# Kernel optimization log

Hardware: AMD Instinct MI355X
Metric: run time of the kernel (lower is better)

The kernel has to match this reference:

```python
import jax, jax.numpy as jnp
import numpy as np

N_NODES = 50000
N_EDGES = 800000
HIDDEN = 128


def setup_inputs() -> dict:
    key = jax.random.key(0)
    k_emb, k_ei, k1, k2, k3, kb1, kb2, kb3 = jax.random.split(key, 8)
    emb = jax.random.normal(k_emb, (N_NODES, HIDDEN), dtype=jnp.float32)
    edge_index = jax.random.randint(k_ei, (2, N_EDGES), 0, N_NODES, dtype=jnp.int64)
    h = HIDDEN
    # MLP([2h, 4h, h, 1]) weights, Kaiming-uniform-ish init
    def lin(k, fan_in, fan_out):
        bound = 1.0 / np.sqrt(fan_in)
        return jax.random.uniform(k, (fan_in, fan_out), jnp.float32, -bound, bound)
    W1 = lin(k1, 2 * h, 4 * h)
    b1 = jax.random.uniform(kb1, (4 * h,), jnp.float32, -1.0 / np.sqrt(2 * h), 1.0 / np.sqrt(2 * h))
    W2 = lin(k2, 4 * h, h)
    b2 = jax.random.uniform(kb2, (h,), jnp.float32, -1.0 / np.sqrt(4 * h), 1.0 / np.sqrt(4 * h))
    W3 = lin(k3, h, 1)
    b3 = jax.random.uniform(kb3, (1,), jnp.float32, -1.0 / np.sqrt(h), 1.0 / np.sqrt(h))
    return {"emb": emb, "edge_index": edge_index,
            "W1": W1, "b1": b1, "W2": W2, "b2": b2, "W3": W3, "b3": b3}


def reference(emb, edge_index, W1, b1, W2, b2, W3, b3):
    # learn_edge_att=True path: gather endpoints, concat, 3-layer MLP
    col, row = edge_index[0], edge_index[1]
    f12 = jnp.concatenate([emb[col], emb[row]], axis=-1)  # [E, 2h]
    x = jax.nn.relu(f12 @ W1 + b1)                         # [E, 4h]
    x = jax.nn.relu(x @ W2 + b2)                           # [E, h]
    att_log_logits = x @ W3 + b3                           # [E, 1]
    return att_log_logits
```

## Files before the change

kernel.cpp:

```cpp
#include <hip/hip_runtime.h>
#include <hip/hip_bf16.h>
#include <stdint.h>

#define N_EDGES   800000
#define N_NODESC  50000
#define HID       128

typedef __attribute__((ext_vector_type(8))) short bf16x8;
typedef __attribute__((ext_vector_type(4))) float f32x4;
typedef __attribute__((ext_vector_type(4))) unsigned int u32x4;

__device__ __forceinline__ short f2bf(float f) {
    union { float f; uint32_t u; } v; v.f = f;
    uint32_t r = v.u + 0x7FFFu + ((v.u >> 16) & 1u);
    return (short)(r >> 16);
}

__device__ __forceinline__ uint32_t packbf2(float lo, float hi) {
    float2 t; t.x = lo; t.y = hi;
    __hip_bfloat162 h = __float22bfloat162_rn(t);
    uint32_t u;
    __builtin_memcpy(&u, &h, 4);
    return u;
}

__device__ __forceinline__ uint32_t addrelu2(uint32_t a, uint32_t b) {
    __hip_bfloat162 ha, hb;
    __builtin_memcpy(&ha, &a, 4);
    __builtin_memcpy(&hb, &b, 4);
    __hip_bfloat162 s = __hadd2(ha, hb);
    uint32_t x;
    __builtin_memcpy(&x, &s, 4);
    uint32_t neg = (x & 0x80008000u) >> 15;
    return x & ~(neg * 0xFFFFu);
}
__device__ __forceinline__ bf16x8 addrelu8(u32x4 p, u32x4 q) {
    u32x4 r;
    #pragma unroll
    for (int j = 0; j < 4; ++j) r[j] = addrelu2(p[j], q[j]);
    bf16x8 out;
    __builtin_memcpy(&out, &r, 16);
    return out;
}

#define PQ_OFF   0UL
#define W1S_OFF  102400000UL
#define W2S_OFF  (W1S_OFF + 262144UL)

__global__ __launch_bounds__(256) void swizzle_kernel(const float* __restrict__ W1,
                                                      const float* __restrict__ W2,
                                                      short* __restrict__ W1s,
                                                      short* __restrict__ W2s) {
    int t = blockIdx.x * 256 + threadIdx.x;
    int lane = t & 63;
    int kq = lane >> 4;
    int nn = lane & 15;
    if (t < 16384) {
        int frag = t >> 6;
        int kc = frag >> 6;
        int nt = frag & 63;
        int n = nt * 16 + nn;
        int kbase = kc * 32 + kq * 8;
        bf16x8 v;
        #pragma unroll
        for (int j = 0; j < 8; ++j) {
            int k = kbase + j;
            float f = (n < 512) ? W1[k * 512 + n] : W1[(128 + k) * 512 + (n - 512)];
            v[j] = f2bf(f);
        }
        *(bf16x8*)(W1s + frag * 512 + lane * 8) = v;
    } else if (t < 24576) {
        int t2 = t - 16384;
        int frag = t2 >> 6;
        int kc = frag >> 3;
        int nt = frag & 7;
        int n = nt * 16 + nn;
        int kbase = kc * 32 + kq * 8;
        bf16x8 v;
        #pragma unroll
        for (int j = 0; j < 8; ++j) v[j] = f2bf(W2[(kbase + j) * HID + n]);
        *(bf16x8*)(W2s + frag * 512 + lane * 8) = v;
    }
}

__global__ __launch_bounds__(256) void precompute_kernel(const float* __restrict__ emb,
                                                         const short* __restrict__ W1s,
                                                         const float* __restrict__ b1,
                                                         short* __restrict__ PQ) {
    __shared__ short tile[4][16][272];
    int lane = threadIdx.x & 63;
    int w = threadIdx.x >> 6;
    int nb = blockIdx.x * 16;
    int m = lane & 15;
    int kq = lane >> 4;

    const float* arow = emb + (size_t)(nb + m) * 128 + kq * 8;

    f32x4 acc[16];
    #pragma unroll
    for (int i = 0; i < 16; ++i) acc[i] = (f32x4){0.f, 0.f, 0.f, 0.f};

    #pragma unroll
    for (int kc = 0; kc < 4; ++kc) {
        f32x4 x0 = *(const f32x4*)(arow + kc * 32);
        f32x4 x1 = *(const f32x4*)(arow + kc * 32 + 4);
        u32x4 au;
        au[0] = packbf2(x0[0], x0[1]); au[1] = packbf2(x0[2], x0[3]);
        au[2] = packbf2(x1[0], x1[1]); au[3] = packbf2(x1[2], x1[3]);
        bf16x8 a;
        __builtin_memcpy(&a, &au, 16);
        #pragma unroll
        for (int nt = 0; nt < 16; ++nt) {
            int frag = kc * 64 + (w * 16 + nt);
            bf16x8 b = *(const bf16x8*)(W1s + frag * 512 + lane * 8);
            acc[nt] = __builtin_amdgcn_mfma_f32_16x16x32_bf16(a, b, acc[nt], 0, 0, 0);
        }
    }

    #pragma unroll
    for (int nt = 0; nt < 16; ++nt) {
        int n = w * 256 + nt * 16 + m;
        float bias = (n < 512) ? b1[n] : 0.0f;
        #pragma unroll
        for (int r = 0; r < 4; ++r)
            tile[w][kq * 4 + r][nt * 16 + m] = f2bf(acc[nt][r] + bias);
    }

    #pragma unroll
    for (int s = 0; s < 8; ++s) {
        int row = s * 2 + (lane >> 5);
        int chunk = lane & 31;
        bf16x8 v = *(const bf16x8*)(&tile[w][row][chunk * 8]);
        *(bf16x8*)(PQ + (size_t)(nb + row) * 1024 + w * 256 + chunk * 8) = v;
    }
}

__global__ __launch_bounds__(256, 2) void edge_kernel(const short* __restrict__ PQ,
                                                      const int* __restrict__ ei,
                                                      const short* __restrict__ W2s,
                                                      const float* __restrict__ b2,
                                                      const float* __restrict__ W3,
                                                      const float* __restrict__ b3,
                                                      float* __restrict__ out) {
    int lane = threadIdx.x & 63;
    int w = threadIdx.x >> 6;
    int e0 = blockIdx.x * 256 + w * 64;
    int m = lane & 15;
    int kq = lane >> 4;

    int idx_c = ei[e0 + lane];
    int idx_r = ei[N_EDGES + e0 + lane];

    const short* pb[4];
    const short* qb[4];
    #pragma unroll
    for (int t = 0; t < 4; ++t) {
        int ce = __shfl(idx_c, t * 16 + m, 64);
        int re = __shfl(idx_r, t * 16 + m, 64);
        pb[t] = PQ + (size_t)ce * 1024 + kq * 8;
        qb[t] = PQ + (size_t)re * 1024 + 512 + kq * 8;
    }

    f32x4 acc[4][8];
    #pragma unroll
    for (int t = 0; t < 4; ++t)
        #pragma unroll
        for (int nt = 0; nt < 8; ++nt) acc[t][nt] = (f32x4){0.f, 0.f, 0.f, 0.f};

    #pragma unroll
    for (int kc = 0; kc < 16; ++kc) {
        u32x4 p[4], q[4];
        #pragma unroll
        for (int t = 0; t < 4; ++t) {
            p[t] = *(const u32x4*)(pb[t] + kc * 32);
            q[t] = *(const u32x4*)(qb[t] + kc * 32);
        }
        bf16x8 b[8];
        #pragma unroll
        for (int nt = 0; nt < 8; ++nt)
            b[nt] = *(const bf16x8*)(W2s + (kc * 8 + nt) * 512 + lane * 8);
        #pragma unroll
        for (int t = 0; t < 4; ++t) {
            bf16x8 a = addrelu8(p[t], q[t]);
            #pragma unroll
            for (int nt = 0; nt < 8; ++nt)
                acc[t][nt] = __builtin_amdgcn_mfma_f32_16x16x32_bf16(a, b[nt], acc[t][nt], 0, 0, 0);
        }
    }

    float b2v[8], w3v[8];
    #pragma unroll
    for (int nt = 0; nt < 8; ++nt) {
        b2v[nt] = b2[nt * 16 + m];
        w3v[nt] = W3[nt * 16 + m];
    }
    float b3s = b3[0];
    #pragma unroll
    for (int t = 0; t < 4; ++t) {
        float partial[4] = {0.f, 0.f, 0.f, 0.f};
        #pragma unroll
        for (int nt = 0; nt < 8; ++nt) {
            #pragma unroll
            for (int r = 0; r < 4; ++r) {
                float x2 = acc[t][nt][r] + b2v[nt];
                x2 = x2 > 0.f ? x2 : 0.f;
                partial[r] += x2 * w3v[nt];
            }
        }
        #pragma unroll
        for (int r = 0; r < 4; ++r) {
            #pragma unroll
            for (int off = 1; off < 16; off <<= 1)
                partial[r] += __shfl_xor(partial[r], off, 64);
            if (m == 0) out[e0 + t * 16 + kq * 4 + r] = partial[r] + b3s;
        }
    }
}

extern "C" void kernel_launch(void* const* d_in, const int* in_sizes, int n_in,
                              void* d_out, int out_size, void* d_ws, size_t ws_size,
                              hipStream_t stream) {
    const float* emb = (const float*)d_in[0];
    const int*   ei  = (const int*)d_in[1];
    const float* W1  = (const float*)d_in[2];
    const float* b1  = (const float*)d_in[3];
    const float* W2  = (const float*)d_in[4];
    const float* b2  = (const float*)d_in[5];
    const float* W3  = (const float*)d_in[6];
    const float* b3  = (const float*)d_in[7];
    float* out = (float*)d_out;

    short* PQ  = (short*)((char*)d_ws + PQ_OFF);
    short* W1s = (short*)((char*)d_ws + W1S_OFF);
    short* W2s = (short*)((char*)d_ws + W2S_OFF);

    swizzle_kernel<<<96, 256, 0, stream>>>(W1, W2, W1s, W2s);
    precompute_kernel<<<N_NODESC / 16, 256, 0, stream>>>(emb, W1s, b1, PQ);
    edge_kernel<<<N_EDGES / 256, 256, 0, stream>>>(PQ, ei, W2s, b2, W3, b3, out);
}
```

Baseline: 400.3 us.

## Bucket-sort edges by endpoint node blocks to improve PQ gather locality

Adds a histogram, a single-block scan and a scatter pass that counting-sort edges into 98x98 buckets keyed by the 512-node blocks of both endpoints. Each edge is packed with its endpoint indices and original id. The edge kernel then processes edges in bucket order and scatters results back through the original id. The aim is better L2/MALL reuse of the 2KB-per-node PQ rows during the random gather. In exchange it adds three kernels, global atomics and a memset, and the output writes become scattered.

```diff
diff --git a/kernel.cpp b/kernel.cpp
--- a/kernel.cpp
+++ b/kernel.cpp
@@ -5,6 +5,7 @@
 #define N_EDGES   800000
 #define N_NODESC  50000
 #define HID       128
+#define NBUCK     (98 * 98)
 
 typedef __attribute__((ext_vector_type(8))) short bf16x8;
 typedef __attribute__((ext_vector_type(4))) float f32x4;
@@ -43,9 +44,12 @@
     return out;
 }
 
-#define PQ_OFF   0UL
-#define W1S_OFF  102400000UL
-#define W2S_OFF  (W1S_OFF + 262144UL)
+#define PQ_OFF    0UL
+#define W1S_OFF   102400000UL
+#define W2S_OFF   (W1S_OFF + 262144UL)
+#define CNT_OFF   (W2S_OFF + 131072UL)
+#define CUR_OFF   (CNT_OFF + 40960UL)
+#define PK_OFF    (CUR_OFF + 40960UL)
 
 __global__ __launch_bounds__(256) void swizzle_kernel(const float* __restrict__ W1,
                                                       const float* __restrict__ W2,
@@ -83,6 +87,69 @@
     }
 }
 
+__global__ __launch_bounds__(256) void hist_kernel(const int* __restrict__ ei,
+                                                   int* __restrict__ cnt) {
+    int e = blockIdx.x * 256 + threadIdx.x;
+    int c = ei[e];
+    int r = ei[N_EDGES + e];
+    atomicAdd(&cnt[(c >> 9) * 98 + (r >> 9)], 1);
+}
+
+__global__ __launch_bounds__(1024) void scan_kernel(const int* __restrict__ cnt,
+                                                    int* __restrict__ cursor) {
+    __shared__ int wsum[16];
+    int tid = threadIdx.x;
+    int lane = tid & 63, wv = tid >> 6;
+    const int CH = (NBUCK + 1023) / 1024;
+    int lo = tid * CH;
+    int local[CH];
+    int s = 0;
+    #pragma unroll
+    for (int i = 0; i < CH; ++i) {
+        int idx = lo + i;
+        int v = (idx < NBUCK) ? cnt[idx] : 0;
+        local[i] = v; s += v;
+    }
+    int run = s;
+    #pragma unroll
+    for (int off = 1; off < 64; off <<= 1) {
+        int t = __shfl_up(run, off, 64);
+        if (lane >= off) run += t;
+    }
+    if (lane == 63) wsum[wv] = run;
+    __syncthreads();
+    if (wv == 0 && lane < 16) {
+        int v = wsum[lane];
+        int r2 = v;
+        #pragma unroll
+        for (int off = 1; off < 16; off <<= 1) {
+            int t = __shfl_up(r2, off, 64);
+            if (lane >= off) r2 += t;
+        }
+        wsum[lane] = r2 - v;
+    }
+    __syncthreads();
+    int base = wsum[wv] + (run - s);
+    #pragma unroll
+    for (int i = 0; i < CH; ++i) {
+        int idx = lo + i;
+        if (idx < NBUCK) { cursor[idx] = base; base += local[i]; }
+    }
+}
+
+__global__ __launch_bounds__(256) void scatter_kernel(const int* __restrict__ ei,
+                                                      int* __restrict__ cursor,
+                                                      uint2* __restrict__ pk) {
+    int e = blockIdx.x * 256 + threadIdx.x;
+    int c = ei[e];
+    int r = ei[N_EDGES + e];
+    int slot = atomicAdd(&cursor[(c >> 9) * 98 + (r >> 9)], 1);
+    uint2 v;
+    v.x = ((uint32_t)c << 16) | (uint32_t)r;
+    v.y = (uint32_t)e;
+    pk[slot] = v;
+}
+
 __global__ __launch_bounds__(256) void precompute_kernel(const float* __restrict__ emb,
                                                          const short* __restrict__ W1s,
                                                          const float* __restrict__ b1,
@@ -136,7 +203,7 @@
 }
 
 __global__ __launch_bounds__(256, 2) void edge_kernel(const short* __restrict__ PQ,
-                                                      const int* __restrict__ ei,
+                                                      const uint2* __restrict__ pk,
                                                       const short* __restrict__ W2s,
                                                       const float* __restrict__ b2,
                                                       const float* __restrict__ W3,
@@ -148,8 +215,10 @@
     int m = lane & 15;
     int kq = lane >> 4;
 
-    int idx_c = ei[e0 + lane];
-    int idx_r = ei[N_EDGES + e0 + lane];
+    uint2 pe = pk[e0 + lane];
+    int idx_c = (int)(pe.x >> 16);
+    int idx_r = (int)(pe.x & 0xFFFFu);
+    int eid   = (int)pe.y;
 
     const short* pb[4];
     const short* qb[4];
@@ -212,7 +281,8 @@
             #pragma unroll
             for (int off = 1; off < 16; off <<= 1)
                 partial[r] += __shfl_xor(partial[r], off, 64);
-            if (m == 0) out[e0 + t * 16 + kq * 4 + r] = partial[r] + b3s;
+            int eo = __shfl(eid, t * 16 + kq * 4 + r, 64);
+            if (m == 0) out[eo] = partial[r] + b3s;
         }
     }
 }
@@ -233,8 +303,15 @@
     short* PQ  = (short*)((char*)d_ws + PQ_OFF);
     short* W1s = (short*)((char*)d_ws + W1S_OFF);
     short* W2s = (short*)((char*)d_ws + W2S_OFF);
-
+    int*   cnt = (int*)((char*)d_ws + CNT_OFF);
+    int*   cur = (int*)((char*)d_ws + CUR_OFF);
+    uint2* pk  = (uint2*)((char*)d_ws + PK_OFF);
+
+    hipMemsetAsync(cnt, 0, NBUCK * sizeof(int), stream);
     swizzle_kernel<<<96, 256, 0, stream>>>(W1, W2, W1s, W2s);
+    hist_kernel<<<N_EDGES / 256, 256, 0, stream>>>(ei, cnt);
+    scan_kernel<<<1, 1024, 0, stream>>>(cnt, cur);
+    scatter_kernel<<<N_EDGES / 256, 256, 0, stream>>>(ei, cur, pk);
     precompute_kernel<<<N_NODESC / 16, 256, 0, stream>>>(emb, W1s, b1, PQ);
-    edge_kernel<<<N_EDGES / 256, 256, 0, stream>>>(PQ, ei, W2s, b2, W3, b3, out);
-}
+    edge_kernel<<<N_EDGES / 256, 256, 0, stream>>>(PQ, pk, W2s, b2, W3, b3, out);
+}
```

Result: slower. 515.7 us (+28.8%).

## Sort edges by source node via cooperative counting sort to improve gather locality

Applied to the files above, without the earlier changes.

Adds a cooperative prep kernel that, besides swizzling the weights, counts edges per source node, prefix-sums the counts across blocks with grid syncs, and scatters packed (col,row,edge id) records into source-sorted order. The edge kernel then reads the sorted records so that P-row gathers for neighbouring edges hit the same rows and get more cache reuse, and it writes each result back to the original edge index. This adds a histogram-and-scatter pass with atomics and four grid-wide syncs on every call, plus scattered output writes, in exchange for more coherent reads from the large PQ table.

```diff
diff --git a/kernel.cpp b/kernel.cpp
--- a/kernel.cpp
+++ b/kernel.cpp
@@ -1,10 +1,16 @@
 #include <hip/hip_runtime.h>
 #include <hip/hip_bf16.h>
+#include <hip/hip_cooperative_groups.h>
 #include <stdint.h>
+
+namespace cg = cooperative_groups;
 
 #define N_EDGES   800000
 #define N_NODESC  50000
 #define HID       128
+
+#define PREP_BLOCKS 782
+#define BPB         64
 
 typedef __attribute__((ext_vector_type(8))) short bf16x8;
 typedef __attribute__((ext_vector_type(4))) float f32x4;
@@ -43,43 +49,107 @@
     return out;
 }
 
-#define PQ_OFF   0UL
-#define W1S_OFF  102400000UL
-#define W2S_OFF  (W1S_OFF + 262144UL)
-
-__global__ __launch_bounds__(256) void swizzle_kernel(const float* __restrict__ W1,
-                                                      const float* __restrict__ W2,
-                                                      short* __restrict__ W1s,
-                                                      short* __restrict__ W2s) {
-    int t = blockIdx.x * 256 + threadIdx.x;
-    int lane = t & 63;
-    int kq = lane >> 4;
-    int nn = lane & 15;
-    if (t < 16384) {
-        int frag = t >> 6;
-        int kc = frag >> 6;
-        int nt = frag & 63;
-        int n = nt * 16 + nn;
-        int kbase = kc * 32 + kq * 8;
-        bf16x8 v;
-        #pragma unroll
-        for (int j = 0; j < 8; ++j) {
-            int k = kbase + j;
-            float f = (n < 512) ? W1[k * 512 + n] : W1[(128 + k) * 512 + (n - 512)];
-            v[j] = f2bf(f);
-        }
-        *(bf16x8*)(W1s + frag * 512 + lane * 8) = v;
-    } else if (t < 24576) {
-        int t2 = t - 16384;
-        int frag = t2 >> 6;
-        int kc = frag >> 3;
-        int nt = frag & 7;
-        int n = nt * 16 + nn;
-        int kbase = kc * 32 + kq * 8;
-        bf16x8 v;
-        #pragma unroll
-        for (int j = 0; j < 8; ++j) v[j] = f2bf(W2[(kbase + j) * HID + n]);
-        *(bf16x8*)(W2s + frag * 512 + lane * 8) = v;
+#define PQ_OFF    0UL
+#define W1S_OFF   102400000UL
+#define W2S_OFF   (W1S_OFF + 262144UL)
+#define CNT_OFF   (W2S_OFF + 131072UL)
+#define CUR_OFF   (CNT_OFF + 200000UL)
+#define BTOT_OFF  (CUR_OFF + 200000UL)
+#define PK_OFF    (BTOT_OFF + 4096UL)
+
+__global__ __launch_bounds__(256) void prep_kernel(const float* __restrict__ W1,
+                                                   const float* __restrict__ W2,
+                                                   short* __restrict__ W1s,
+                                                   short* __restrict__ W2s,
+                                                   const int* __restrict__ ei,
+                                                   int* __restrict__ cnt,
+                                                   int* __restrict__ btot,
+                                                   int* __restrict__ cursor,
+                                                   uint2* __restrict__ pk) {
+    cg::grid_group grid = cg::this_grid();
+    __shared__ int red[256];
+    int tid = threadIdx.x;
+    int b = blockIdx.x;
+    int gid = b * 256 + tid;
+    const int GSTRIDE = PREP_BLOCKS * 256;
+
+    {
+        int lane = gid & 63;
+        int kq = lane >> 4;
+        int nn = lane & 15;
+        if (gid < 16384) {
+            int frag = gid >> 6;
+            int kc = frag >> 6;
+            int nt = frag & 63;
+            int n = nt * 16 + nn;
+            int kbase = kc * 32 + kq * 8;
+            bf16x8 v;
+            #pragma unroll
+            for (int j = 0; j < 8; ++j) {
+                int k = kbase + j;
+                float f = (n < 512) ? W1[k * 512 + n] : W1[(128 + k) * 512 + (n - 512)];
+                v[j] = f2bf(f);
+            }
+            *(bf16x8*)(W1s + frag * 512 + lane * 8) = v;
+        } else if (gid < 24576) {
+            int t2 = gid - 16384;
+            int frag = t2 >> 6;
+            int kc = frag >> 3;
+            int nt = frag & 7;
+            int n = nt * 16 + nn;
+            int kbase = kc * 32 + kq * 8;
+            bf16x8 v;
+            #pragma unroll
+            for (int j = 0; j < 8; ++j) v[j] = f2bf(W2[(kbase + j) * HID + n]);
+            *(bf16x8*)(W2s + frag * 512 + lane * 8) = v;
+        }
+    }
+    if (gid < N_NODESC) cnt[gid] = 0;
+    grid.sync();
+
+    for (int e = gid; e < N_EDGES; e += GSTRIDE)
+        atomicAdd(&cnt[ei[e]], 1);
+    grid.sync();
+
+    if (tid < 64) {
+        int idx = b * BPB + tid;
+        int v = (idx < N_NODESC) ? cnt[idx] : 0;
+        #pragma unroll
+        for (int off = 32; off; off >>= 1) v += __shfl_down(v, off, 64);
+        if (tid == 0) btot[b] = v;
+    }
+    grid.sync();
+
+    int part = 0;
+    for (int j = tid; j < b; j += 256) part += btot[j];
+    red[tid] = part;
+    __syncthreads();
+    #pragma unroll
+    for (int s = 128; s; s >>= 1) {
+        if (tid < s) red[tid] += red[tid + s];
+        __syncthreads();
+    }
+    if (tid < 64) {
+        int idx = b * BPB + tid;
+        int v = (idx < N_NODESC) ? cnt[idx] : 0;
+        int run = v;
+        #pragma unroll
+        for (int off = 1; off < 64; off <<= 1) {
+            int t = __shfl_up(run, off, 64);
+            if (tid >= off) run += t;
+        }
+        if (idx < N_NODESC) cursor[idx] = red[0] + run - v;
+    }
+    grid.sync();
+
+    for (int e = gid; e < N_EDGES; e += GSTRIDE) {
+        int c = ei[e];
+        int r = ei[N_EDGES + e];
+        int slot = atomicAdd(&cursor[c], 1);
+        uint2 v;
+        v.x = ((uint32_t)c << 16) | (uint32_t)r;
+        v.y = (uint32_t)e;
+        pk[slot] = v;
     }
 }
 
@@ -112,8 +182,8 @@
         #pragma unroll
         for (int nt = 0; nt < 16; ++nt) {
             int frag = kc * 64 + (w * 16 + nt);
-            bf16x8 b = *(const bf16x8*)(W1s + frag * 512 + lane * 8);
-            acc[nt] = __builtin_amdgcn_mfma_f32_16x16x32_bf16(a, b, acc[nt], 0, 0, 0);
+            bf16x8 bb = *(const bf16x8*)(W1s + frag * 512 + lane * 8);
+            acc[nt] = __builtin_amdgcn_mfma_f32_16x16x32_bf16(a, bb, acc[nt], 0, 0, 0);
         }
     }
 
@@ -136,7 +206,7 @@
 }
 
 __global__ __launch_bounds__(256, 2) void edge_kernel(const short* __restrict__ PQ,
-                                                      const int* __restrict__ ei,
+                                                      const uint2* __restrict__ pk,
                                                       const short* __restrict__ W2s,
                                                       const float* __restrict__ b2,
                                                       const float* __restrict__ W3,
@@ -148,8 +218,10 @@
     int m = lane & 15;
     int kq = lane >> 4;
 
-    int idx_c = ei[e0 + lane];
-    int idx_r = ei[N_EDGES + e0 + lane];
+    uint2 pe = pk[e0 + lane];
+    int idx_c = (int)(pe.x >> 16);
+    int idx_r = (int)(pe.x & 0xFFFFu);
+    int eid   = (int)pe.y;
 
     const short* pb[4];
     const short* qb[4];
@@ -212,7 +284,8 @@
             #pragma unroll
             for (int off = 1; off < 16; off <<= 1)
                 partial[r] += __shfl_xor(partial[r], off, 64);
-            if (m == 0) out[e0 + t * 16 + kq * 4 + r] = partial[r] + b3s;
+            int eo = __shfl(eid, t * 16 + kq * 4 + r, 64);
+            if (m == 0) out[eo] = partial[r] + b3s;
         }
     }
 }
@@ -230,11 +303,18 @@
     const float* b3  = (const float*)d_in[7];
     float* out = (float*)d_out;
 
-    short* PQ  = (short*)((char*)d_ws + PQ_OFF);
-    short* W1s = (short*)((char*)d_ws + W1S_OFF);
-    short* W2s = (short*)((char*)d_ws + W2S_OFF);
-
-    swizzle_kernel<<<96, 256, 0, stream>>>(W1, W2, W1s, W2s);
+    short* PQ   = (short*)((char*)d_ws + PQ_OFF);
+    short* W1s  = (short*)((char*)d_ws + W1S_OFF);
+    short* W2s  = (short*)((char*)d_ws + W2S_OFF);
+    int*   cnt  = (int*)((char*)d_ws + CNT_OFF);
+    int*   cur  = (int*)((char*)d_ws + CUR_OFF);
+    int*   btot = (int*)((char*)d_ws + BTOT_OFF);
+    uint2* pk   = (uint2*)((char*)d_ws + PK_OFF);
+
+    void* args[] = {(void*)&W1, (void*)&W2, (void*)&W1s, (void*)&W2s,
+                    (void*)&ei, (void*)&cnt, (void*)&btot, (void*)&cur, (void*)&pk};
+    hipLaunchCooperativeKernel((const void*)prep_kernel,
+                               dim3(PREP_BLOCKS), dim3(256), args, 0, stream);
     precompute_kernel<<<N_NODESC / 16, 256, 0, stream>>>(emb, W1s, b1, PQ);
-    edge_kernel<<<N_EDGES / 256, 256, 0, stream>>>(PQ, ei, W2s, b2, W3, b3, out);
-}
+    edge_kernel<<<N_EDGES / 256, 256, 0, stream>>>(PQ, pk, W2s, b2, W3, b3, out);
+}
```

New measurement: 809.0 us. 2.02x slower.
